# Kernel tuning notes

Measured on AMD Instinct MI355X. Metric: run time of the kernel, lower is better.

## Reference

```python
import jax, jax.numpy as jnp
import numpy as np

T, N, E, D, OUT, L = 12, 10000, 160000, 128, 64, 2


def setup_inputs() -> dict:
    key = jax.random.key(0)
    ks = jax.random.split(key, 8)
    s = 1.0 / np.sqrt(D)
    x = jax.random.normal(ks[0], (T, N, D), jnp.float32)
    hidden_states = jax.random.normal(ks[1], (L, N, D), jnp.float32)
    src = jax.random.randint(ks[2], (E,), 0, N, dtype=jnp.int32)
    dst = jax.random.randint(ks[3], (E,), 0, N, dtype=jnp.int32)
    W_self = jax.random.normal(ks[4], (L, 6, D, D), jnp.float32) * s
    W_neigh = jax.random.normal(ks[5], (L, 6, D, D), jnp.float32) * s
    b = jnp.zeros((L, 6, D), jnp.float32)
    W_out = jax.random.normal(ks[6], (D, OUT), jnp.float32) * s
    b_out = jnp.zeros((OUT,), jnp.float32)
    return dict(x=x, hidden_states=hidden_states, W_self=W_self, W_neigh=W_neigh,
                b=b, W_out=W_out, b_out=b_out, src=src, dst=dst)


def reference(x, hidden_states, W_self, W_neigh, b, W_out, b_out, src, dst):
    n_nodes = x.shape[1]
    deg = jax.ops.segment_sum(jnp.ones_like(dst, jnp.float32), dst, num_segments=n_nodes)
    deg_inv = jnp.where(deg > 0, 1.0 / deg, 0.0)[:, None]  # [N,1]

    def agg(f):  # mean over in-neighbors (DGL update_all copy_u + mean)
        return jax.ops.segment_sum(f[src], dst, num_segments=n_nodes) * deg_inv

    # agg_seq=True: original concatenates all timesteps and does one update_all;
    # mean is per-feature, so this equals per-timestep neighbor means, vmapped.
    hN_all = jax.vmap(agg)(x)  # [T,N,D]

    def net(f, fN, i, Ws, Wn, bl):  # SAGE-mean style message-passing net
        return f @ Ws[i] + fN @ Wn[i] + bl[i]

    def cell(xin, h, hN_x, Ws, Wn, bl):
        if hN_x is None:
            hN_x = agg(xin)
        hN_h = agg(h)
        r = jax.nn.sigmoid(net(xin, hN_x, 0, Ws, Wn, bl) + net(h, hN_h, 1, Ws, Wn, bl))
        u = jax.nn.sigmoid(net(xin, hN_x, 2, Ws, Wn, bl) + net(h, hN_h, 3, Ws, Wn, bl))
        c = jnp.tanh(net(xin, hN_x, 4, Ws, Wn, bl) + net(h, hN_h, 5, Ws, Wn, bl))
        return u * h + (1.0 - u) * c  # note: r*h is dead code in the source

    def step(hidden, inp_t):
        x_t, hN_t = inp_t
        cur, hN = x_t, hN_t
        new_h = []
        for j in range(L):  # small fixed depth
            cur = cell(cur, hidden[j], hN, W_self[j], W_neigh[j], b[j])
            new_h.append(cur)
            hN = None  # h_N only used by first layer (as in source)
        out = cur @ W_out + b_out
        return jnp.stack(new_h), out

    hidden_final, outputs = jax.lax.scan(step, hidden_states, (x, hN_all))
    return outputs, hidden_final
```

## Files before the change

### kernel.cpp

```cpp
#include <hip/hip_runtime.h>

typedef unsigned short u16;
typedef unsigned int   u32;
typedef __attribute__((ext_vector_type(4))) float f32x4;
typedef __attribute__((ext_vector_type(8))) short s16x8;

#define TT 12
#define NN 10000
#define EE 160000
#define DD 128
#define OO 64

__device__ __forceinline__ u16 f2bf(float f) {
  union { float f; u32 u; } x; x.f = f;
  u32 r = x.u + 0x7FFFu + ((x.u >> 16) & 1u);
  return (u16)(r >> 16);
}
__device__ __forceinline__ float bf2f(u16 v) {
  union { u32 u; float f; } x; x.u = (u32)v << 16; return x.f;
}

__device__ __forceinline__ void gload_lds16(const u16* g, u16* l) {
  __builtin_amdgcn_global_load_lds(
      (const __attribute__((address_space(1))) u32*)(const void*)g,
      (__attribute__((address_space(3))) u32*)(void*)l, 16, 0, 0);
}

__global__ __launch_bounds__(256) void prep_kernel(
    const float* __restrict__ x, const float* __restrict__ hs,
    const int* __restrict__ dst,
    const float* __restrict__ Wself, const float* __restrict__ Wneigh,
    const float* __restrict__ b, const float* __restrict__ Wout,
    u16* __restrict__ xb, float* __restrict__ h0f, u16* __restrict__ hb0,
    float* __restrict__ h1f, u16* __restrict__ hb1,
    int* __restrict__ deg, u16* __restrict__ Wp,
    float* __restrict__ biasbuf, u16* __restrict__ WoT,
    int nx8, int nh8half, int E) {
  int gid = blockIdx.x * 256 + threadIdx.x;
  const int NWP = 2 * 256 * 512;
  const int NPACK = NWP + 64 * 128 + 512;
  int cvtXEnd = NPACK + nx8;
  int cvtHEnd = cvtXEnd + 2 * nh8half;
  int cntEnd  = cvtHEnd + E;
  if (gid < NPACK) {
    int pg = gid;
    if (pg < NWP) {
      int cc = pg & 127;
      int kd = (pg >> 7) & 127;
      int gm = (pg >> 14) & 7;
      int j  = pg >> 17;
      int gate = 2 + (gm & 3);
      int neigh = gm >> 2;
      const float* M = neigh ? Wneigh : Wself;
      float v = M[(((j * 6) + gate) * 128 + kd) * 128 + cc];
      int c = cc + ((gate >= 4) ? 128 : 0);
      int seg = (gate & 1) * 2 + neigh;
      int k = seg * 128 + kd;
      int kc = k >> 6, k6 = k & 63;
      int ksw = ((k6 & ~7) ^ ((c & 7) << 3)) | (k6 & 7);
      Wp[(size_t)j * 131072 + c * 512 + kc * 64 + ksw] = f2bf(v);
    } else if (pg < NWP + 64 * 128) {
      int i = pg - NWP;
      int c = i >> 7, k = i & 127;
      WoT[i] = f2bf(Wout[k * OO + c]);
    } else {
      int i = pg - NWP - 64 * 128;
      int j = i >> 8, g = (i >> 7) & 1, d = i & 127;
      int g1 = g ? 4 : 2, g2 = g ? 5 : 3;
      biasbuf[i] = b[(j * 6 + g1) * 128 + d] + b[(j * 6 + g2) * 128 + d];
    }
  } else if (gid < cvtXEnd) {
    int i8 = gid - NPACK;
    float4 va = *(const float4*)(x + (size_t)i8 * 8);
    float4 vb = *(const float4*)(x + (size_t)i8 * 8 + 4);
    uint4 p;
    p.x = (u32)f2bf(va.x) | ((u32)f2bf(va.y) << 16);
    p.y = (u32)f2bf(va.z) | ((u32)f2bf(va.w) << 16);
    p.z = (u32)f2bf(vb.x) | ((u32)f2bf(vb.y) << 16);
    p.w = (u32)f2bf(vb.z) | ((u32)f2bf(vb.w) << 16);
    *(uint4*)(xb + (size_t)i8 * 8) = p;
  } else if (gid < cvtHEnd) {
    int j = gid - cvtXEnd;
    int half = (j >= nh8half);
    int jj = half ? j - nh8half : j;
    float4 va = ((const float4*)hs)[(size_t)j * 2];
    float4 vb = ((const float4*)hs)[(size_t)j * 2 + 1];
    float* fdst = half ? h1f : h0f;
    u16*   bdst = half ? hb1 : hb0;
    ((float4*)fdst)[(size_t)jj * 2]     = va;
    ((float4*)fdst)[(size_t)jj * 2 + 1] = vb;
    uint4 p;
    p.x = (u32)f2bf(va.x) | ((u32)f2bf(va.y) << 16);
    p.y = (u32)f2bf(va.z) | ((u32)f2bf(va.w) << 16);
    p.z = (u32)f2bf(vb.x) | ((u32)f2bf(vb.y) << 16);
    p.w = (u32)f2bf(vb.z) | ((u32)f2bf(vb.w) << 16);
    ((uint4*)bdst)[jj] = p;
  } else if (gid < cntEnd) {
    int e = gid - cvtHEnd;
    atomicAdd(&deg[dst[e]], 1);
  }
}

__global__ __launch_bounds__(1024) void scan_kernel(const int* __restrict__ deg,
                                                    int* __restrict__ offs,
                                                    float* __restrict__ dinv, int n) {
  __shared__ int lds_deg[10240];
  __shared__ int wsum[16];
  int tid = threadIdx.x;
  for (int i = tid; i < 10240; i += 1024) lds_deg[i] = (i < n) ? deg[i] : 0;
  __syncthreads();
  int base = tid * 10;
  int loc[10];
  int s = 0;
  #pragma unroll
  for (int k = 0; k < 10; ++k) { loc[k] = s; s += lds_deg[base + k]; }
  int lane = tid & 63;
  int incl = s;
  #pragma unroll
  for (int d = 1; d < 64; d <<= 1) {
    int t2 = __shfl_up(incl, d);
    if (lane >= d) incl += t2;
  }
  int wid = tid >> 6;
  if (lane == 63) wsum[wid] = incl;
  __syncthreads();
  int wpre = 0;
  for (int k = 0; k < wid; ++k) wpre += wsum[k];
  int excl = wpre + incl - s;
  #pragma unroll
  for (int k = 0; k < 10; ++k) {
    int idx = base + k;
    if (idx < n) {
      int d0 = lds_deg[idx];
      offs[idx] = excl + loc[k];
      dinv[idx] = (d0 > 0) ? 1.0f / (float)d0 : 0.0f;
    }
  }
  if (tid == 1023) offs[n] = excl + s;
}

__global__ __launch_bounds__(256) void fill_kernel(const int* __restrict__ src,
                                                   const int* __restrict__ dst,
                                                   const int* __restrict__ offs,
                                                   int* __restrict__ cursor,
                                                   int* __restrict__ csr, int E) {
  int e = blockIdx.x * 256 + threadIdx.x;
  if (e >= E) return;
  int d = dst[e];
  int pos = atomicAdd(&cursor[d], 1);
  csr[offs[d] + pos] = src[e] * 64;
}

__device__ __forceinline__ void acc4(u32 vx, u32 vy, float& a, float& b, float& c, float& d) {
  a += bf2f((u16)vx); b += bf2f((u16)(vx >> 16));
  c += bf2f((u16)vy); d += bf2f((u16)(vy >> 16));
}

__device__ __forceinline__ void agg_one2(const int* __restrict__ offs,
                                         const int* __restrict__ csr,
                                         const float* __restrict__ dinv,
                                         const u32* __restrict__ S,
                                         u32* __restrict__ O,
                                         int node, int lane) {
  int nu = __builtin_amdgcn_readfirstlane(node);
  int e0 = offs[nu], e1 = offs[nu + 1];
  float di = dinv[nu];
  int half = lane >> 5;
  int col = (lane & 31) * 2;
  float a0 = 0, b0 = 0, c0 = 0, d0 = 0, a1 = 0, b1 = 0, c1 = 0, d1 = 0;
  int e = e0;
  for (; e + 8 <= e1; e += 8) {
    int p0 = csr[e],     p1 = csr[e + 1], p2 = csr[e + 2], p3 = csr[e + 3];
    int p4 = csr[e + 4], p5 = csr[e + 5], p6 = csr[e + 6], p7 = csr[e + 7];
    uint2 v0 = *(const uint2*)(S + (half ? p1 : p0) + col);
    uint2 v1 = *(const uint2*)(S + (half ? p3 : p2) + col);
    uint2 v2 = *(const uint2*)(S + (half ? p5 : p4) + col);
    uint2 v3 = *(const uint2*)(S + (half ? p7 : p6) + col);
    acc4(v0.x, v0.y, a0, b0, c0, d0);
    acc4(v1.x, v1.y, a1, b1, c1, d1);
    acc4(v2.x, v2.y, a0, b0, c0, d0);
    acc4(v3.x, v3.y, a1, b1, c1, d1);
  }
  if (e + 4 <= e1) {
    int p0 = csr[e], p1 = csr[e + 1], p2 = csr[e + 2], p3 = csr[e + 3];
    uint2 v0 = *(const uint2*)(S + (half ? p1 : p0) + col);
    uint2 v1 = *(const uint2*)(S + (half ? p3 : p2) + col);
    acc4(v0.x, v0.y, a0, b0, c0, d0);
    acc4(v1.x, v1.y, a1, b1, c1, d1);
    e += 4;
  }
  if (e + 2 <= e1) {
    int p0 = csr[e], p1 = csr[e + 1];
    uint2 v0 = *(const uint2*)(S + (half ? p1 : p0) + col);
    acc4(v0.x, v0.y, a0, b0, c0, d0);
    e += 2;
  }
  if (e < e1) {
    uint2 v0 = *(const uint2*)(S + csr[e] + col);
    if (!half) acc4(v0.x, v0.y, a1, b1, c1, d1);
  }
  float sa = a0 + a1, sb = b0 + b1, sc = c0 + c1, sd = d0 + d1;
  sa += __shfl_down(sa, 32);
  sb += __shfl_down(sb, 32);
  sc += __shfl_down(sc, 32);
  sd += __shfl_down(sd, 32);
  if (!half) {
    uint2 o;
    o.x = (u32)f2bf(sa * di) | ((u32)f2bf(sb * di) << 16);
    o.y = (u32)f2bf(sc * di) | ((u32)f2bf(sd * di) << 16);
    *(uint2*)(O + (size_t)nu * 64 + col) = o;
  }
}

__global__ __launch_bounds__(256) void aggx_kernel(const int* __restrict__ offs,
                                                   const int* __restrict__ csr,
                                                   const float* __restrict__ dinv,
                                                   const u16* __restrict__ xb,
                                                   u16* __restrict__ axb,
                                                   const u16* __restrict__ hb0,
                                                   u16* __restrict__ ah0, int N) {
  int id = blockIdx.x;
  const u32* S; u32* O; int grp;
  if (id < 20000) {
    int t = id & 7; grp = id >> 3;
    S = (const u32*)xb + (size_t)t * N * 64; O = (u32*)axb + (size_t)t * N * 64;
  } else if (id < 30000) {
    int j = id - 20000;
    int slot = j & 7;
    int t = 8 + (slot & 3);
    grp = (slot >> 2) * 1250 + (j >> 3);
    S = (const u32*)xb + (size_t)t * N * 64; O = (u32*)axb + (size_t)t * N * 64;
  } else {
    grp = id - 30000;
    S = (const u32*)hb0; O = (u32*)ah0;
  }
  int node = grp * 4 + (threadIdx.x >> 6);
  if (node >= N) return;
  agg_one2(offs, csr, dinv, S, O, node, threadIdx.x & 63);
}

__global__ __launch_bounds__(256) void aggdual_kernel(const int* __restrict__ offs,
                                                      const int* __restrict__ csr,
                                                      const float* __restrict__ dinv,
                                                      const u16* __restrict__ s0,
                                                      const u16* __restrict__ s1,
                                                      u16* __restrict__ o0,
                                                      u16* __restrict__ o1, int N) {
  int b = blockIdx.x;
  int srcsel = (b >> 2) & 1;
  int idx = (b >> 3) * 4 + (b & 3);
  int node = idx * 4 + (threadIdx.x >> 6);
  if (node >= N) return;
  const u32* S = (const u32*)(srcsel ? s1 : s0);
  u32* O = (u32*)(srcsel ? o1 : o0);
  agg_one2(offs, csr, dinv, S, O, node, threadIdx.x & 63);
}

template <int MODE>
__device__ __forceinline__ void cell_body(char* __restrict__ smem, int row0, int tid,
    const u16* __restrict__ s0, const u16* __restrict__ s1,
    const u16* __restrict__ s2, const u16* __restrict__ s3,
    const u16* __restrict__ W, const float* __restrict__ bias,
    const float* __restrict__ hin, float* __restrict__ hout, u16* __restrict__ hbout,
    const u16* __restrict__ WoT, const float* __restrict__ bout,
    float* __restrict__ outp, int N) {
  u16* As = (u16*)smem;
  u16* Bs = (u16*)(smem + 8192);
  const u16* srcs[4] = {s0, s1, s2, s3};
  int lane = tid & 63, w = tid >> 6;
  int wr = w & 3, wc = w >> 2;

  f32x4 accU[4], accC[4];
  #pragma unroll
  for (int n = 0; n < 4; ++n) { accU[n] = (f32x4){0,0,0,0}; accC[n] = (f32x4){0,0,0,0}; }

  #pragma unroll
  for (int kc = 0; kc < 8; ++kc) {
    {
      int r = tid >> 3, k8 = (tid & 7) * 8;
      int k8s = k8 ^ ((r & 7) << 3);
      const u16* g = srcs[kc >> 1] + (size_t)(row0 + r) * DD + (kc & 1) * 64 + k8s;
      gload_lds16(g, As + (tid & ~63) * 8);
    }
    #pragma unroll
    for (int it = 0; it < 4; ++it) {
      int id = it * 512 + tid;
      const u16* g = W + (id >> 3) * 512 + kc * 64 + (id & 7) * 8;
      gload_lds16(g, Bs + (it * 512 + (tid & ~63)) * 8);
    }
    __syncthreads();
    #pragma unroll
    for (int ks = 0; ks < 2; ++ks) {
      int arow = wr * 16 + (lane & 15);
      int abyte = (arow * 128 + ks * 64 + (lane >> 4) * 16) ^ ((arow & 7) << 4);
      s16x8 af = *(const s16x8*)((char*)As + abyte);
      #pragma unroll
      for (int n = 0; n < 4; ++n) {
        int cu = wc * 64 + n * 16 + (lane & 15);
        int bub = (cu * 128 + ks * 64 + (lane >> 4) * 16) ^ ((cu & 7) << 4);
        s16x8 bu = *(const s16x8*)((char*)Bs + bub);
        accU[n] = __builtin_amdgcn_mfma_f32_16x16x32_bf16(af, bu, accU[n], 0, 0, 0);
        int cc = cu + 128;
        int bcb = (cc * 128 + ks * 64 + (lane >> 4) * 16) ^ ((cc & 7) << 4);
        s16x8 bc = *(const s16x8*)((char*)Bs + bcb);
        accC[n] = __builtin_amdgcn_mfma_f32_16x16x32_bf16(af, bc, accC[n], 0, 0, 0);
      }
    }
    __syncthreads();
  }

  #pragma unroll
  for (int n = 0; n < 4; ++n) {
    int col = wc * 64 + n * 16 + (lane & 15);
    float bu = bias[col], bc = bias[128 + col];
    #pragma unroll
    for (int r = 0; r < 4; ++r) {
      int row = row0 + wr * 16 + (lane >> 4) * 4 + r;
      if (row < N) {
        float u = 1.0f / (1.0f + __expf(-(accU[n][r] + bu)));
        float cg = tanhf(accC[n][r] + bc);
        size_t idx = (size_t)row * DD + col;
        float hn = u * hin[idx] + (1.0f - u) * cg;
        hout[idx] = hn;
        u16 hnb = f2bf(hn);
        hbout[idx] = hnb;
        if constexpr (MODE == 2) {
          int rl = row - row0;
          int hbyte = (rl * 256 + col * 2) ^ ((rl & 7) << 4);
          *(u16*)(smem + hbyte) = hnb;
        }
      }
    }
  }
  if constexpr (MODE == 2) {
    #pragma unroll
    for (int it = 0; it < 2; ++it) {
      int id = it * 512 + tid;
      int c = id >> 4, kc8 = (id & 15) * 8;
      uint4 v = *(const uint4*)(WoT + c * 128 + kc8);
      int byte = (c * 256 + kc8 * 2) ^ ((c & 7) << 4);
      *(uint4*)(smem + 16384 + byte) = v;
    }
    __syncthreads();
    f32x4 ao[2] = {};
    #pragma unroll
    for (int ks = 0; ks < 4; ++ks) {
      int arow = wr * 16 + (lane & 15);
      int abyte = (arow * 256 + ks * 64 + (lane >> 4) * 16) ^ ((arow & 7) << 4);
      s16x8 af = *(const s16x8*)(smem + abyte);
      #pragma unroll
      for (int n = 0; n < 2; ++n) {
        int co = wc * 32 + n * 16 + (lane & 15);
        int bbyte = (co * 256 + ks * 64 + (lane >> 4) * 16) ^ ((co & 7) << 4);
        s16x8 bf = *(const s16x8*)(smem + 16384 + bbyte);
        ao[n] = __builtin_amdgcn_mfma_f32_16x16x32_bf16(af, bf, ao[n], 0, 0, 0);
      }
    }
    #pragma unroll
    for (int n = 0; n < 2; ++n) {
      int co = wc * 32 + n * 16 + (lane & 15);
      float bb = bout[co];
      #pragma unroll
      for (int r = 0; r < 4; ++r) {
        int row = row0 + wr * 16 + (lane >> 4) * 4 + r;
        if (row < N) outp[(size_t)row * OO + co] = ao[n][r] + bb;
      }
    }
  }
}

__global__ __launch_bounds__(512) void cell0_kernel(const u16* __restrict__ xbt,
                                                    const u16* __restrict__ axbt,
                                                    const u16* __restrict__ hb0c,
                                                    const u16* __restrict__ ah0,
                                                    const u16* __restrict__ W,
                                                    const float* __restrict__ bias,
                                                    const float* __restrict__ h0in,
                                                    float* __restrict__ h0out,
                                                    u16* __restrict__ hb0out, int N) {
  __shared__ __align__(16) char smem[40960];
  cell_body<3>(smem, blockIdx.x * 64, threadIdx.x, xbt, axbt, hb0c, ah0,
               W, bias, h0in, h0out, hb0out, nullptr, nullptr, nullptr, N);
}

template <int WITHC0>
__global__ __launch_bounds__(512) void step_kernel(const u16* __restrict__ xbn,
                                                   const u16* __restrict__ axbn,
                                                   const u16* __restrict__ hb0c,
                                                   const u16* __restrict__ ah0,
                                                   const u16* __restrict__ hb1r,
                                                   const u16* __restrict__ ah1,
                                                   const u16* __restrict__ Wp,
                                                   const float* __restrict__ biasbuf,
                                                   const float* __restrict__ h1in,
                                                   float* __restrict__ h1out,
                                                   u16* __restrict__ hb1w,
                                                   const float* __restrict__ h0in,
                                                   float* __restrict__ h0out,
                                                   u16* __restrict__ hb0out,
                                                   const u16* __restrict__ WoT,
                                                   const float* __restrict__ bout,
                                                   float* __restrict__ outp, int N) {
  __shared__ __align__(16) char smem[40960];
  int bx = blockIdx.x;
  int role = WITHC0 ? (bx & 1) : 0;
  int row0 = (WITHC0 ? (bx >> 1) : bx) * 64;
  if (role == 0) {
    cell_body<2>(smem, row0, threadIdx.x, hb0c, ah0, hb1r, ah1,
                 Wp + 131072, biasbuf + 256,
                 h1in, h1out, hb1w, WoT, bout, outp, N);
  } else {
    cell_body<3>(smem, row0, threadIdx.x, xbn, axbn, hb0c, ah0,
                 Wp, biasbuf,
                 h0in, h0out, hb0out, nullptr, nullptr, nullptr, N);
  }
}

extern "C" void kernel_launch(void* const* d_in, const int* in_sizes, int n_in,
                              void* d_out, int out_size, void* d_ws, size_t ws_size,
                              hipStream_t stream) {
  const float* x      = (const float*)d_in[0];
  const float* hs     = (const float*)d_in[1];
  const float* Wself  = (const float*)d_in[2];
  const float* Wneigh = (const float*)d_in[3];
  const float* b      = (const float*)d_in[4];
  const float* Wout   = (const float*)d_in[5];
  const float* bout   = (const float*)d_in[6];
  const int*   src    = (const int*)d_in[7];
  const int*   dst    = (const int*)d_in[8];
  float* out = (float*)d_out;

  const int N = NN, E = EE, D = DD, T = TT;

  char* ws = (char*)d_ws;
  size_t off = 0;
  auto alloc = [&](size_t bytes) -> void* {
    void* p = ws + off;
    off = (off + bytes + 255) & ~(size_t)255;
    return p;
  };
  int*   deg     = (int*)alloc(N * 4);
  int*   offs    = (int*)alloc((N + 1) * 4);
  int*   cursor  = (int*)alloc(N * 4);
  int*   csr     = (int*)alloc(E * 4);
  float* dinv    = (float*)alloc(N * 4);
  u16*   Wp      = (u16*)alloc(2 * 256 * 512 * 2);
  float* biasbuf = (float*)alloc(512 * 4);
  u16*   WoT     = (u16*)alloc(64 * 128 * 2);
  float* h0A     = (float*)alloc((size_t)N * D * 4);
  float* h0B     = (float*)alloc((size_t)N * D * 4);
  float* h1f     = (float*)alloc((size_t)N * D * 4);
  u16*   hb0A    = (u16*)alloc((size_t)N * D * 2);
  u16*   hb0B    = (u16*)alloc((size_t)N * D * 2);
  u16*   hb1     = (u16*)alloc((size_t)N * D * 2);
  u16*   ah0b    = (u16*)alloc((size_t)N * D * 2);
  u16*   ah1b    = (u16*)alloc((size_t)N * D * 2);
  u16*   xb      = (u16*)alloc((size_t)T * N * D * 2);
  u16*   axb     = (u16*)alloc((size_t)T * N * D * 2);
  (void)alloc(65536);

  float* h0f[2] = {h0A, h0B};
  u16*   hb0[2] = {hb0A, hb0B};
  float* hid0 = out + (size_t)T * N * OO;
  float* hid1 = hid0 + (size_t)N * D;

  hipMemsetAsync(deg, 0, N * 4, stream);
  hipMemsetAsync(cursor, 0, N * 4, stream);
  {
    int nx8 = T * N * D / 8, nh8half = N * D / 8;
    int NPACK = 2 * 256 * 512 + 64 * 128 + 512;
    int tot = NPACK + nx8 + 2 * nh8half + E;
    prep_kernel<<<(tot + 255) / 256, 256, 0, stream>>>(
        x, hs, dst, Wself, Wneigh, b, Wout,
        xb, h0A, hb0A, h1f, hb1, deg, Wp, biasbuf, WoT, nx8, nh8half, E);
  }
  scan_kernel<<<1, 1024, 0, stream>>>(deg, offs, dinv, N);
  fill_kernel<<<(E + 255) / 256, 256, 0, stream>>>(src, dst, offs, cursor, csr, E);

  int aggGrid = (N + 3) / 4;
  int mmGrid  = (N + 63) / 64;

  aggx_kernel<<<32500, 256, 0, stream>>>(offs, csr, dinv, xb, axb, hb0A, ah0b, N);
  cell0_kernel<<<mmGrid, 512, 0, stream>>>(xb, axb, hb0A, ah0b, Wp, biasbuf,
                                           h0A, h0B, hb0B, N);

  for (int t = 0; t < T; ++t) {
    u16* cur = hb0[(t + 1) & 1];
    aggdual_kernel<<<2 * aggGrid, 256, 0, stream>>>(offs, csr, dinv, cur, hb1,
                                                    ah0b, ah1b, N);
    if (t < T - 1) {
      float* h0o = (t == T - 2) ? hid0 : h0f[t & 1];
      step_kernel<1><<<2 * mmGrid, 512, 0, stream>>>(
          xb + (size_t)(t + 1) * N * D, axb + (size_t)(t + 1) * N * D,
          cur, ah0b, hb1, ah1b, Wp, biasbuf,
          h1f, h1f, hb1,
          h0f[(t + 1) & 1], h0o, hb0[t & 1],
          WoT, bout, out + (size_t)t * N * OO, N);
    } else {
      step_kernel<0><<<mmGrid, 512, 0, stream>>>(
          nullptr, nullptr,
          cur, ah0b, hb1, ah1b, Wp, biasbuf,
          h1f, hid1, hb1, nullptr, nullptr, nullptr,
          WoT, bout, out + (size_t)t * N * OO, N);
    }
  }
}
```

Baseline: 620.6 us.

## Double-buffer LDS tiles in cell GEMM and widen aggregation gather unroll

The cell GEMM now keeps two LDS stages, so the global-to-LDS loads for the next K chunk are issued before the MFMAs on the current chunk, with one wait and barrier per iteration instead of two syncs. This doubles shared memory per block to 80 KB, which may lower occupancy. The neighbor aggregation loop now handles 16 edges per iteration and loads only each half-wave's own CSR indices, giving more gathers in flight per wave at some register cost.

```diff
diff --git a/kernel.cpp b/kernel.cpp
--- a/kernel.cpp
+++ b/kernel.cpp
@@ -169,29 +169,59 @@
   int col = (lane & 31) * 2;
   float a0 = 0, b0 = 0, c0 = 0, d0 = 0, a1 = 0, b1 = 0, c1 = 0, d1 = 0;
   int e = e0;
-  for (; e + 8 <= e1; e += 8) {
-    int p0 = csr[e],     p1 = csr[e + 1], p2 = csr[e + 2], p3 = csr[e + 3];
-    int p4 = csr[e + 4], p5 = csr[e + 5], p6 = csr[e + 6], p7 = csr[e + 7];
-    uint2 v0 = *(const uint2*)(S + (half ? p1 : p0) + col);
-    uint2 v1 = *(const uint2*)(S + (half ? p3 : p2) + col);
-    uint2 v2 = *(const uint2*)(S + (half ? p5 : p4) + col);
-    uint2 v3 = *(const uint2*)(S + (half ? p7 : p6) + col);
+  for (; e + 16 <= e1; e += 16) {
+    int q0 = csr[e + (half ? 1 : 0)];
+    int q1 = csr[e + (half ? 3 : 2)];
+    int q2 = csr[e + (half ? 5 : 4)];
+    int q3 = csr[e + (half ? 7 : 6)];
+    int q4 = csr[e + (half ? 9 : 8)];
+    int q5 = csr[e + (half ? 11 : 10)];
+    int q6 = csr[e + (half ? 13 : 12)];
+    int q7 = csr[e + (half ? 15 : 14)];
+    uint2 v0 = *(const uint2*)(S + q0 + col);
+    uint2 v1 = *(const uint2*)(S + q1 + col);
+    uint2 v2 = *(const uint2*)(S + q2 + col);
+    uint2 v3 = *(const uint2*)(S + q3 + col);
+    uint2 v4 = *(const uint2*)(S + q4 + col);
+    uint2 v5 = *(const uint2*)(S + q5 + col);
+    uint2 v6 = *(const uint2*)(S + q6 + col);
+    uint2 v7 = *(const uint2*)(S + q7 + col);
     acc4(v0.x, v0.y, a0, b0, c0, d0);
     acc4(v1.x, v1.y, a1, b1, c1, d1);
     acc4(v2.x, v2.y, a0, b0, c0, d0);
     acc4(v3.x, v3.y, a1, b1, c1, d1);
+    acc4(v4.x, v4.y, a0, b0, c0, d0);
+    acc4(v5.x, v5.y, a1, b1, c1, d1);
+    acc4(v6.x, v6.y, a0, b0, c0, d0);
+    acc4(v7.x, v7.y, a1, b1, c1, d1);
+  }
+  if (e + 8 <= e1) {
+    int q0 = csr[e + (half ? 1 : 0)];
+    int q1 = csr[e + (half ? 3 : 2)];
+    int q2 = csr[e + (half ? 5 : 4)];
+    int q3 = csr[e + (half ? 7 : 6)];
+    uint2 v0 = *(const uint2*)(S + q0 + col);
+    uint2 v1 = *(const uint2*)(S + q1 + col);
+    uint2 v2 = *(const uint2*)(S + q2 + col);
+    uint2 v3 = *(const uint2*)(S + q3 + col);
+    acc4(v0.x, v0.y, a0, b0, c0, d0);
+    acc4(v1.x, v1.y, a1, b1, c1, d1);
+    acc4(v2.x, v2.y, a0, b0, c0, d0);
+    acc4(v3.x, v3.y, a1, b1, c1, d1);
+    e += 8;
   }
   if (e + 4 <= e1) {
-    int p0 = csr[e], p1 = csr[e + 1], p2 = csr[e + 2], p3 = csr[e + 3];
-    uint2 v0 = *(const uint2*)(S + (half ? p1 : p0) + col);
-    uint2 v1 = *(const uint2*)(S + (half ? p3 : p2) + col);
+    int q0 = csr[e + (half ? 1 : 0)];
+    int q1 = csr[e + (half ? 3 : 2)];
+    uint2 v0 = *(const uint2*)(S + q0 + col);
+    uint2 v1 = *(const uint2*)(S + q1 + col);
     acc4(v0.x, v0.y, a0, b0, c0, d0);
     acc4(v1.x, v1.y, a1, b1, c1, d1);
     e += 4;
   }
   if (e + 2 <= e1) {
-    int p0 = csr[e], p1 = csr[e + 1];
-    uint2 v0 = *(const uint2*)(S + (half ? p1 : p0) + col);
+    int q0 = csr[e + (half ? 1 : 0)];
+    uint2 v0 = *(const uint2*)(S + q0 + col);
     acc4(v0.x, v0.y, a0, b0, c0, d0);
     e += 2;
   }
@@ -264,8 +294,6 @@
     const float* __restrict__ hin, float* __restrict__ hout, u16* __restrict__ hbout,
     const u16* __restrict__ WoT, const float* __restrict__ bout,
     float* __restrict__ outp, int N) {
-  u16* As = (u16*)smem;
-  u16* Bs = (u16*)(smem + 8192);
   const u16* srcs[4] = {s0, s1, s2, s3};
   int lane = tid & 63, w = tid >> 6;
   int wr = w & 3, wc = w >> 2;
@@ -274,39 +302,54 @@
   #pragma unroll
   for (int n = 0; n < 4; ++n) { accU[n] = (f32x4){0,0,0,0}; accC[n] = (f32x4){0,0,0,0}; }
 
-  #pragma unroll
-  for (int kc = 0; kc < 8; ++kc) {
+  auto STAGE = [&](int kc, int bsel) {
+    char* base = smem + bsel * 40960;
     {
       int r = tid >> 3, k8 = (tid & 7) * 8;
       int k8s = k8 ^ ((r & 7) << 3);
       const u16* g = srcs[kc >> 1] + (size_t)(row0 + r) * DD + (kc & 1) * 64 + k8s;
-      gload_lds16(g, As + (tid & ~63) * 8);
+      gload_lds16(g, (u16*)base + (tid & ~63) * 8);
     }
     #pragma unroll
     for (int it = 0; it < 4; ++it) {
       int id = it * 512 + tid;
       const u16* g = W + (id >> 3) * 512 + kc * 64 + (id & 7) * 8;
-      gload_lds16(g, Bs + (it * 512 + (tid & ~63)) * 8);
-    }
-    __syncthreads();
+      gload_lds16(g, (u16*)(base + 8192) + (it * 512 + (tid & ~63)) * 8);
+    }
+  };
+
+  STAGE(0, 0);
+  asm volatile("s_waitcnt vmcnt(0)" ::: "memory");
+  __builtin_amdgcn_s_barrier();
+  asm volatile("" ::: "memory");
+
+  int bsel = 0;
+  #pragma unroll
+  for (int kc = 0; kc < 8; ++kc) {
+    if (kc < 7) STAGE(kc + 1, bsel ^ 1);
+    char* As = smem + bsel * 40960;
+    char* Bs = As + 8192;
     #pragma unroll
     for (int ks = 0; ks < 2; ++ks) {
       int arow = wr * 16 + (lane & 15);
       int abyte = (arow * 128 + ks * 64 + (lane >> 4) * 16) ^ ((arow & 7) << 4);
-      s16x8 af = *(const s16x8*)((char*)As + abyte);
+      s16x8 af = *(const s16x8*)(As + abyte);
       #pragma unroll
       for (int n = 0; n < 4; ++n) {
         int cu = wc * 64 + n * 16 + (lane & 15);
         int bub = (cu * 128 + ks * 64 + (lane >> 4) * 16) ^ ((cu & 7) << 4);
-        s16x8 bu = *(const s16x8*)((char*)Bs + bub);
+        s16x8 bu = *(const s16x8*)(Bs + bub);
         accU[n] = __builtin_amdgcn_mfma_f32_16x16x32_bf16(af, bu, accU[n], 0, 0, 0);
         int cc = cu + 128;
         int bcb = (cc * 128 + ks * 64 + (lane >> 4) * 16) ^ ((cc & 7) << 4);
-        s16x8 bc = *(const s16x8*)((char*)Bs + bcb);
+        s16x8 bc = *(const s16x8*)(Bs + bcb);
         accC[n] = __builtin_amdgcn_mfma_f32_16x16x32_bf16(af, bc, accC[n], 0, 0, 0);
       }
     }
-    __syncthreads();
+    asm volatile("s_waitcnt vmcnt(0)" ::: "memory");
+    __builtin_amdgcn_s_barrier();
+    asm volatile("" ::: "memory");
+    bsel ^= 1;
   }
 
   #pragma unroll
@@ -378,7 +421,7 @@
                                                     const float* __restrict__ h0in,
                                                     float* __restrict__ h0out,
                                                     u16* __restrict__ hb0out, int N) {
-  __shared__ __align__(16) char smem[40960];
+  __shared__ __align__(16) char smem[81920];
   cell_body<3>(smem, blockIdx.x * 64, threadIdx.x, xbt, axbt, hb0c, ah0,
                W, bias, h0in, h0out, hb0out, nullptr, nullptr, nullptr, N);
 }
@@ -401,7 +444,7 @@
                                                    const u16* __restrict__ WoT,
                                                    const float* __restrict__ bout,
                                                    float* __restrict__ outp, int N) {
-  __shared__ __align__(16) char smem[40960];
+  __shared__ __align__(16) char smem[81920];
   int bx = blockIdx.x;
   int role = WITHC0 ? (bx & 1) : 0;
   int row0 = (WITHC0 ? (bx >> 1) : bx) * 64;
```

New measurement: 622.6 us. Within noise of the previous version (+0.3%).
